# Optimization experiments

Hardware: AMD Instinct MI355X
Metric: run time of the kernel (lower is better)

Reference implementation:

```python
import jax, jax.numpy as jnp
import numpy as np

B, N, IN_DIM, H, D = 8, 128, 512, 8, 64  # batch, nodes, in_dim, heads, head_dim


def setup_inputs() -> dict:
    key = jax.random.key(0)
    ks = jax.random.split(key, 11)
    s = 0.02
    return {
        "h": jax.random.normal(ks[0], (B, N, IN_DIM), jnp.float32),
        "e": jax.random.normal(ks[1], (B, N, N, IN_DIM), jnp.float32),
        "k_RW": jax.random.uniform(ks[2], (B, N, N), jnp.float32),
        # Linear params stored as [in, out] (transpose of torch convention)
        "Wq": jax.random.normal(ks[3], (IN_DIM, H * D), jnp.float32) * s,
        "bq": jax.random.normal(ks[4], (H * D,), jnp.float32) * s,
        "Wk": jax.random.normal(ks[5], (IN_DIM, H * D), jnp.float32) * s,
        "bk": jax.random.normal(ks[6], (H * D,), jnp.float32) * s,
        "We": jax.random.normal(ks[7], (IN_DIM, H * D), jnp.float32) * s,
        "be": jax.random.normal(ks[8], (H * D,), jnp.float32) * s,
        "Wv": jax.random.normal(ks[9], (IN_DIM, H * D), jnp.float32) * s,
        "bv": jax.random.normal(ks[10], (H * D,), jnp.float32) * s,
    }


def reference(h, e, k_RW, Wq, bq, Wk, bk, We, be, Wv, bv):
    b, n = h.shape[0], h.shape[1]
    Q = (h @ Wq + bq).reshape(b, n, H, D)                       # bihd
    K = (h @ Wk + bk).reshape(b, n, H, D) * (float(D) ** -0.5)  # bjhd, scaled
    V = (h @ Wv + bv).reshape(b, n, H, D).transpose(0, 2, 1, 3)  # bhjd
    E = (e @ We + be).reshape(b, n, n, H, D)                    # bijhd
    # multiplicative edge-modulated attention scores
    scores = jnp.einsum('bihd,bjhd,bijhd->bhij', Q, K, E)
    scores = jnp.exp(jnp.clip(scores, -5.0, 5.0))
    scores = scores * k_RW[:, None, :, :]                       # adaptive edge PE
    denom = jnp.maximum(scores.sum(-1, keepdims=True), 1e-6)
    out = (scores @ V) / denom                                  # bhid
    return out.transpose(0, 2, 1, 3).reshape(b, n, H * D)
```

## Files before the change

kernel.cpp:

```cpp
#include <hip/hip_runtime.h>
#include <hip/hip_bf16.h>

#define BB    8
#define NNODE 128
#define CIN   512
#define HH    8
#define DDIM  64
#define HD    512

typedef float f32x4 __attribute__((ext_vector_type(4)));
typedef short bf16x8 __attribute__((ext_vector_type(8)));
typedef unsigned int u32x4 __attribute__((ext_vector_type(4)));

#define AS1 __attribute__((address_space(1)))
#define AS3 __attribute__((address_space(3)))

static __device__ __forceinline__ unsigned short f2bf(float f) {
    unsigned int x = __float_as_uint(f);
    x = x + 0x7FFFu + ((x >> 16) & 1u);
    return (unsigned short)(x >> 16);
}

static __device__ __forceinline__ bf16x8 pack8(f32x4 a, f32x4 b) {
    bf16x8 r;
    r[0] = (short)f2bf(a[0]); r[1] = (short)f2bf(a[1]);
    r[2] = (short)f2bf(a[2]); r[3] = (short)f2bf(a[3]);
    r[4] = (short)f2bf(b[0]); r[5] = (short)f2bf(b[1]);
    r[6] = (short)f2bf(b[2]); r[7] = (short)f2bf(b[3]);
    return r;
}

static __device__ __forceinline__ bf16x8 cvt8(f32x4 a, f32x4 b) {
    union { u32x4 u; bf16x8 h8; } cv;
    asm("v_cvt_pk_bf16_f32 %0, %1, %2" : "=v"(cv.u[0]) : "v"(a[0]), "v"(a[1]));
    asm("v_cvt_pk_bf16_f32 %0, %1, %2" : "=v"(cv.u[1]) : "v"(a[2]), "v"(a[3]));
    asm("v_cvt_pk_bf16_f32 %0, %1, %2" : "=v"(cv.u[2]) : "v"(b[0]), "v"(b[1]));
    asm("v_cvt_pk_bf16_f32 %0, %1, %2" : "=v"(cv.u[3]) : "v"(b[2]), "v"(b[3]));
    return cv.h8;
}

__global__ __launch_bounds__(256) void k_wt(
    const float* __restrict__ Wq, const float* __restrict__ Wk,
    const float* __restrict__ Wv,
    unsigned short* __restrict__ WT)
{
    __shared__ unsigned short tile[64][72];
    const int cb = blockIdx.x;
    const int hb = blockIdx.y;
    const int m  = blockIdx.z;
    const float* W = (m == 0) ? Wq : (m == 1) ? Wk : Wv;
    const int t = threadIdx.x;

#pragma unroll
    for (int it = 0; it < 4; ++it) {
        int row = it * 16 + (t >> 4);
        int col = (t & 15) * 4;
        f32x4 v = *reinterpret_cast<const f32x4*>(W + (size_t)(cb * 64 + row) * HD + hb * 64 + col);
        tile[row][col + 0] = f2bf(v[0]);
        tile[row][col + 1] = f2bf(v[1]);
        tile[row][col + 2] = f2bf(v[2]);
        tile[row][col + 3] = f2bf(v[3]);
    }
    __syncthreads();

#pragma unroll
    for (int it = 0; it < 4; ++it) {
        int hd = it * 16 + (t >> 4);
        int c  = (t & 15) * 4;
        unsigned long long pk =
            (unsigned long long)(unsigned short)tile[c + 0][hd] |
            ((unsigned long long)(unsigned short)tile[c + 1][hd] << 16) |
            ((unsigned long long)(unsigned short)tile[c + 2][hd] << 32) |
            ((unsigned long long)(unsigned short)tile[c + 3][hd] << 48);
        *reinterpret_cast<unsigned long long*>(
            &WT[((size_t)(m + 1) * HD + hb * 64 + hd) * CIN + cb * 64 + c]) = pk;
    }
}

__global__ __launch_bounds__(256) void k_qkv(
    const float* __restrict__ hin,
    const unsigned short* __restrict__ WT,
    const float* __restrict__ bq, const float* __restrict__ bk, const float* __restrict__ bv,
    float* __restrict__ Qo, float* __restrict__ Ko, float* __restrict__ Vo)
{
    __shared__ unsigned short hs[64][520];
    const int rt = blockIdx.x;
    const int ct = blockIdx.y;
    const int m  = blockIdx.z;
    const int t  = threadIdx.x;
    const int w  = t >> 6;
    const int l  = t & 63;
    const int g  = l >> 4;
    const int c15 = l & 15;
    const float* bias = (m == 0) ? bq : (m == 1) ? bk : bv;
    float* Out = (m == 0) ? Qo : (m == 1) ? Ko : Vo;
    const unsigned short* Wm = WT + (size_t)(m + 1) * HD * CIN;
    const int rowbase = rt * 64;
    const int colbase = ct * 64;

#pragma unroll
    for (int q = 0; q < 32; ++q) {
        int f = q * 1024 + t * 4;
        int row = f >> 9;
        int c = f & 511;
        f32x4 hv = *reinterpret_cast<const f32x4*>(hin + (size_t)(rowbase + row) * CIN + c);
        unsigned long long pk =
            (unsigned long long)f2bf(hv[0]) |
            ((unsigned long long)f2bf(hv[1]) << 16) |
            ((unsigned long long)f2bf(hv[2]) << 32) |
            ((unsigned long long)f2bf(hv[3]) << 48);
        *reinterpret_cast<unsigned long long*>(&hs[row][c]) = pk;
    }
    __syncthreads();

    f32x4 acc[4];
#pragma unroll
    for (int nf = 0; nf < 4; ++nf) acc[nf] = (f32x4){0.f, 0.f, 0.f, 0.f};

#pragma unroll
    for (int kt = 0; kt < 16; ++kt) {
        bf16x8 afr = *reinterpret_cast<const bf16x8*>(&hs[w * 16 + c15][kt * 32 + g * 8]);
#pragma unroll
        for (int nf = 0; nf < 4; ++nf) {
            const unsigned short* wp = Wm + (size_t)(colbase + nf * 16 + c15) * CIN + kt * 32 + g * 8;
            bf16x8 bfr = *reinterpret_cast<const bf16x8*>(wp);
            acc[nf] = __builtin_amdgcn_mfma_f32_16x16x32_bf16(afr, bfr, acc[nf], 0, 0, 0);
        }
    }

    const float scale = (m == 1) ? 0.125f : 1.0f;
#pragma unroll
    for (int nf = 0; nf < 4; ++nf) {
        int col = colbase + nf * 16 + c15;
        float bv_ = bias[col];
#pragma unroll
        for (int r = 0; r < 4; ++r) {
            int row = rowbase + w * 16 + g * 4 + r;
            Out[(size_t)row * HD + col] = (acc[nf][r] + bv_) * scale;
        }
    }
}

__global__ __launch_bounds__(256) void k_wtb(
    const float* __restrict__ We, unsigned short* __restrict__ WTB)
{
    const int h  = blockIdx.x;
    const int ct = blockIdx.y;
    const int t  = threadIdx.x;
#pragma unroll
    for (int it = 0; it < 2; ++it) {
        int s  = it * 256 + t;
        int kt = s >> 8, nf = (s >> 6) & 3, l = s & 63;
        int c0 = ct * 64 + kt * 32 + (l >> 4) * 8;
        int hd = h * 64 + nf * 16 + (l & 15);
        bf16x8 v;
#pragma unroll
        for (int i = 0; i < 8; ++i)
            v[i] = (short)f2bf(We[(size_t)(c0 + i) * HD + hd]);
        size_t off = ((size_t)(h * 8 + ct) * 8 + kt * 4 + nf) * 512 + l * 8;
        *reinterpret_cast<bf16x8*>(&WTB[off]) = v;
    }
}

__global__ __launch_bounds__(512, 1) void k_main(
    const float* __restrict__ e, const float* __restrict__ k_RW,
    const unsigned short* __restrict__ WTB, const float* __restrict__ be,
    const float* __restrict__ Qw, const float* __restrict__ Kw,
    const float* __restrict__ Vw, float* __restrict__ out)
{
    __shared__ float e_s[3 * 8192];
    __shared__ float s_lds[8][128];

    const int bx = blockIdx.x;
    const int bi = (bx & 7) * 128 + (bx >> 3);
    const int b  = bi >> 7;
    const int t  = threadIdx.x;
    const int h  = t >> 6;
    const int l  = t & 63;
    const int g  = l >> 4;
    const int c15 = l & 15;

    const float* ebase = e + (size_t)bi * NNODE * CIN;

    float q_l[4], be_l[4];
#pragma unroll
    for (int nf = 0; nf < 4; ++nf) {
        q_l[nf]  = Qw[(size_t)bi * HD + h * 64 + nf * 16 + c15];
        be_l[nf] = be[h * 64 + nf * 16 + c15];
    }

    f32x4 acc[8][4];
#pragma unroll
    for (int mf = 0; mf < 8; ++mf)
#pragma unroll
        for (int nf = 0; nf < 4; ++nf)
            acc[mf][nf] = (f32x4){0.f, 0.f, 0.f, 0.f};

    const int s00 = (((g * 2) + 0) ^ c15) << 4;
    const int s01 = (((g * 2) + 1) ^ c15) << 4;
    const int s10 = ((8 + (g * 2) + 0) ^ c15) << 4;
    const int s11 = ((8 + (g * 2) + 1) ^ c15) << 4;

#define STAGE(TT) do {                                                          \
        _Pragma("unroll")                                                       \
        for (int q_ = 0; q_ < 4; ++q_) {                                        \
            const int key_ = q_ * 4 + g;                                        \
            const float* src_ = ebase + (size_t)(h * 16 + key_) * CIN           \
                                + (TT) * 64 + ((c15 ^ key_) << 2);              \
            __builtin_amdgcn_global_load_lds(                                   \
                (const AS1 unsigned int*)src_,                                  \
                (AS3 unsigned int*)((char*)&e_s[0] + ((TT) % 3) * 32768         \
                                    + h * 4096 + q_ * 1024), 16, 0, 0);         \
        }                                                                       \
    } while (0)

#define LOADB(CT, B) do {                                                       \
        const unsigned short* bp_ = WTB + ((size_t)(h * 8 + (CT)) * 8) * 512 + l * 8; \
        _Pragma("unroll")                                                       \
        for (int f_ = 0; f_ < 8; ++f_)                                          \
            B[f_] = *reinterpret_cast<const bf16x8*>(bp_ + f_ * 512);           \
    } while (0)

#define COMPUTE(CT, BC) do {                                                    \
        const char* ebuf_ = (const char*)&e_s[0] + ((CT) % 3) * 32768;          \
        _Pragma("unroll")                                                       \
        for (int mf_ = 0; mf_ < 8; ++mf_) {                                     \
            const char* rp_ = ebuf_ + (mf_ * 16 + c15) * 256;                   \
            bf16x8 a0_ = cvt8(*(const f32x4*)(rp_ + s00),                       \
                              *(const f32x4*)(rp_ + s01));                      \
            bf16x8 a1_ = cvt8(*(const f32x4*)(rp_ + s10),                       \
                              *(const f32x4*)(rp_ + s11));                      \
            _Pragma("unroll")                                                   \
            for (int nf_ = 0; nf_ < 4; ++nf_) {                                 \
                acc[mf_][nf_] = __builtin_amdgcn_mfma_f32_16x16x32_bf16(        \
                    a0_, BC[nf_], acc[mf_][nf_], 0, 0, 0);                      \
                acc[mf_][nf_] = __builtin_amdgcn_mfma_f32_16x16x32_bf16(        \
                    a1_, BC[4 + nf_], acc[mf_][nf_], 0, 0, 0);                  \
            }                                                                   \
        }                                                                       \
    } while (0)

#define PHASE(CT, BC, BN) do {                                                  \
        if ((CT) < 7) { asm volatile("s_waitcnt vmcnt(4)" ::: "memory"); }      \
        else          { asm volatile("s_waitcnt vmcnt(0)" ::: "memory"); }      \
        __builtin_amdgcn_sched_barrier(0);                                      \
        __builtin_amdgcn_s_barrier();                                           \
        __builtin_amdgcn_sched_barrier(0);                                      \
        if ((CT) < 7) { LOADB((CT) + 1, BN); }                                  \
        __builtin_amdgcn_sched_barrier(0);                                      \
        if ((CT) < 6) { STAGE((CT) + 2); }                                      \
        __builtin_amdgcn_sched_barrier(0);                                      \
        COMPUTE(CT, BC);                                                        \
    } while (0)

    bf16x8 B0[8], B1[8];

    STAGE(0);
    LOADB(0, B0);
    STAGE(1);
    __builtin_amdgcn_sched_barrier(0);

    PHASE(0, B0, B1);
    PHASE(1, B1, B0);
    PHASE(2, B0, B1);
    PHASE(3, B1, B0);
    PHASE(4, B0, B1);
    PHASE(5, B1, B0);
    PHASE(6, B0, B1);
    PHASE(7, B1, B0);
#undef PHASE
#undef COMPUTE
#undef LOADB
#undef STAGE

    const float* Kb  = Kw + (size_t)b * NNODE * HD;
    const float* krw = k_RW + (size_t)bi * NNODE;
#pragma unroll
    for (int mf = 0; mf < 8; ++mf) {
#pragma unroll
        for (int r = 0; r < 4; ++r) {
            int j = mf * 16 + g * 4 + r;
            float s = 0.f;
#pragma unroll
            for (int nf = 0; nf < 4; ++nf) {
                float kv = Kb[(size_t)j * HD + h * 64 + nf * 16 + c15];
                s += (acc[mf][nf][r] + be_l[nf]) * q_l[nf] * kv;
            }
            s += __shfl_xor(s, 1);
            s += __shfl_xor(s, 2);
            s += __shfl_xor(s, 4);
            s += __shfl_xor(s, 8);
            if (c15 == 0)
                s_lds[h][j] = __expf(fminf(fmaxf(s, -5.f), 5.f)) * krw[j];
        }
    }

    const float* Vb = Vw + (size_t)b * NNODE * HD + h * 64 + l;
    float o = 0.f, den = 0.f;
#pragma unroll 4
    for (int jl = 0; jl < NNODE; ++jl) {
        float sv = s_lds[h][jl];
        o = fmaf(sv, Vb[(size_t)jl * HD], o);
        den += sv;
    }
    out[(size_t)bi * HD + h * 64 + l] = o / fmaxf(den, 1e-6f);
}

extern "C" void kernel_launch(void* const* d_in, const int* in_sizes, int n_in,
                              void* d_out, int out_size, void* d_ws, size_t ws_size,
                              hipStream_t stream) {
    const float* hin = (const float*)d_in[0];
    const float* e   = (const float*)d_in[1];
    const float* krw = (const float*)d_in[2];
    const float* Wq  = (const float*)d_in[3];
    const float* bq  = (const float*)d_in[4];
    const float* Wk  = (const float*)d_in[5];
    const float* bk  = (const float*)d_in[6];
    const float* We  = (const float*)d_in[7];
    const float* be  = (const float*)d_in[8];
    const float* Wv  = (const float*)d_in[9];
    const float* bv  = (const float*)d_in[10];
    float* out = (float*)d_out;

    char* ws = (char*)d_ws;
    unsigned short* WT  = (unsigned short*)ws;
    float* Q  = (float*)(ws + (2ull << 20));
    float* K  = (float*)(ws + (4ull << 20));
    float* V  = (float*)(ws + (6ull << 20));
    unsigned short* WTB = (unsigned short*)(ws + (8ull << 20));

    k_wt  <<<dim3(8, 8, 3), dim3(256), 0, stream>>>(Wq, Wk, Wv, WT);
    k_wtb <<<dim3(8, 8),    dim3(256), 0, stream>>>(We, WTB);
    k_qkv <<<dim3(16, 8, 3), dim3(256), 0, stream>>>(hin, WT, bq, bk, bv, Q, K, V);
    k_main<<<dim3(1024), dim3(512), 0, stream>>>(e, krw, WTB, be, Q, K, V, out);
}
```

Before: 220.3 us.

## Split main kernel over key halves with partial sums and normalization pass

Each (b,i) row is now handled by two blocks, each covering 64 of the 128 key nodes. Smaller LDS staging and fewer accumulators allow two blocks per CU. The blocks write partial numerators and denominators, and a new k_norm kernel combines them. The We B-fragment load drops from double buffering to a single buffer loaded within each phase, which exposes its latency. The change aims to raise occupancy and hide the memory stream of e, at the cost of an extra launch and a small workspace round-trip.

```diff
diff --git a/kernel.cpp b/kernel.cpp
--- a/kernel.cpp
+++ b/kernel.cpp
@@ -19,15 +19,6 @@
     unsigned int x = __float_as_uint(f);
     x = x + 0x7FFFu + ((x >> 16) & 1u);
     return (unsigned short)(x >> 16);
-}
-
-static __device__ __forceinline__ bf16x8 pack8(f32x4 a, f32x4 b) {
-    bf16x8 r;
-    r[0] = (short)f2bf(a[0]); r[1] = (short)f2bf(a[1]);
-    r[2] = (short)f2bf(a[2]); r[3] = (short)f2bf(a[3]);
-    r[4] = (short)f2bf(b[0]); r[5] = (short)f2bf(b[1]);
-    r[6] = (short)f2bf(b[2]); r[7] = (short)f2bf(b[3]);
-    return r;
 }
 
 static __device__ __forceinline__ bf16x8 cvt8(f32x4 a, f32x4 b) {
@@ -162,69 +153,63 @@
     }
 }
 
-__global__ __launch_bounds__(512, 1) void k_main(
+__global__ __launch_bounds__(512, 2) void k_main(
     const float* __restrict__ e, const float* __restrict__ k_RW,
     const unsigned short* __restrict__ WTB, const float* __restrict__ be,
     const float* __restrict__ Qw, const float* __restrict__ Kw,
-    const float* __restrict__ Vw, float* __restrict__ out)
-{
-    __shared__ float e_s[3 * 8192];
-    __shared__ float s_lds[8][128];
-
-    const int bx = blockIdx.x;
-    const int bi = (bx & 7) * 128 + (bx >> 3);
-    const int b  = bi >> 7;
-    const int t  = threadIdx.x;
-    const int h  = t >> 6;
-    const int l  = t & 63;
-    const int g  = l >> 4;
-    const int c15 = l & 15;
-
-    const float* ebase = e + (size_t)bi * NNODE * CIN;
-
-    float q_l[4], be_l[4];
-#pragma unroll
-    for (int nf = 0; nf < 4; ++nf) {
-        q_l[nf]  = Qw[(size_t)bi * HD + h * 64 + nf * 16 + c15];
-        be_l[nf] = be[h * 64 + nf * 16 + c15];
-    }
-
-    f32x4 acc[8][4];
-#pragma unroll
-    for (int mf = 0; mf < 8; ++mf)
+    const float* __restrict__ Vw, float* __restrict__ PN, float* __restrict__ PD)
+{
+    __shared__ float e_s[3 * 4096];
+    __shared__ float s_lds[8][64];
+
+    const int bx   = blockIdx.x;
+    const int bi   = bx >> 1;
+    const int half = bx & 1;
+    const int b    = bi >> 7;
+    const int t    = threadIdx.x;
+    const int h    = t >> 6;
+    const int l    = t & 63;
+    const int g    = l >> 4;
+    const int c15  = l & 15;
+
+    const float* ebase = e + ((size_t)bi * NNODE + half * 64) * CIN;
+
+    f32x4 acc[4][4];
+#pragma unroll
+    for (int mf = 0; mf < 4; ++mf)
 #pragma unroll
         for (int nf = 0; nf < 4; ++nf)
             acc[mf][nf] = (f32x4){0.f, 0.f, 0.f, 0.f};
 
-    const int s00 = (((g * 2) + 0) ^ c15) << 4;
-    const int s01 = (((g * 2) + 1) ^ c15) << 4;
-    const int s10 = ((8 + (g * 2) + 0) ^ c15) << 4;
-    const int s11 = ((8 + (g * 2) + 1) ^ c15) << 4;
+    const int s00 = ((g * 2 + 0) ^ c15) << 4;
+    const int s01 = ((g * 2 + 1) ^ c15) << 4;
+    const int s10 = ((8 + g * 2 + 0) ^ c15) << 4;
+    const int s11 = ((8 + g * 2 + 1) ^ c15) << 4;
 
 #define STAGE(TT) do {                                                          \
         _Pragma("unroll")                                                       \
-        for (int q_ = 0; q_ < 4; ++q_) {                                        \
-            const int key_ = q_ * 4 + g;                                        \
-            const float* src_ = ebase + (size_t)(h * 16 + key_) * CIN           \
+        for (int q_ = 0; q_ < 2; ++q_) {                                        \
+            const int key_ = ((h & 1) << 3) + q_ * 4 + g;                       \
+            const float* src_ = ebase + (size_t)(h * 8 + q_ * 4 + g) * CIN      \
                                 + (TT) * 64 + ((c15 ^ key_) << 2);              \
             __builtin_amdgcn_global_load_lds(                                   \
                 (const AS1 unsigned int*)src_,                                  \
-                (AS3 unsigned int*)((char*)&e_s[0] + ((TT) % 3) * 32768         \
-                                    + h * 4096 + q_ * 1024), 16, 0, 0);         \
+                (AS3 unsigned int*)((char*)&e_s[0] + ((TT) % 3) * 16384         \
+                                    + h * 2048 + q_ * 1024), 16, 0, 0);         \
         }                                                                       \
     } while (0)
 
-#define LOADB(CT, B) do {                                                       \
+#define LOADB(CT) do {                                                          \
         const unsigned short* bp_ = WTB + ((size_t)(h * 8 + (CT)) * 8) * 512 + l * 8; \
         _Pragma("unroll")                                                       \
         for (int f_ = 0; f_ < 8; ++f_)                                          \
-            B[f_] = *reinterpret_cast<const bf16x8*>(bp_ + f_ * 512);           \
+            wB[f_] = *reinterpret_cast<const bf16x8*>(bp_ + f_ * 512);          \
     } while (0)
 
-#define COMPUTE(CT, BC) do {                                                    \
-        const char* ebuf_ = (const char*)&e_s[0] + ((CT) % 3) * 32768;          \
+#define COMPUTE(CT) do {                                                        \
+        const char* ebuf_ = (const char*)&e_s[0] + ((CT) % 3) * 16384;          \
         _Pragma("unroll")                                                       \
-        for (int mf_ = 0; mf_ < 8; ++mf_) {                                     \
+        for (int mf_ = 0; mf_ < 4; ++mf_) {                                     \
             const char* rp_ = ebuf_ + (mf_ * 16 + c15) * 256;                   \
             bf16x8 a0_ = cvt8(*(const f32x4*)(rp_ + s00),                       \
                               *(const f32x4*)(rp_ + s01));                      \
@@ -233,57 +218,64 @@
             _Pragma("unroll")                                                   \
             for (int nf_ = 0; nf_ < 4; ++nf_) {                                 \
                 acc[mf_][nf_] = __builtin_amdgcn_mfma_f32_16x16x32_bf16(        \
-                    a0_, BC[nf_], acc[mf_][nf_], 0, 0, 0);                      \
+                    a0_, wB[nf_], acc[mf_][nf_], 0, 0, 0);                      \
                 acc[mf_][nf_] = __builtin_amdgcn_mfma_f32_16x16x32_bf16(        \
-                    a1_, BC[4 + nf_], acc[mf_][nf_], 0, 0, 0);                  \
+                    a1_, wB[4 + nf_], acc[mf_][nf_], 0, 0, 0);                  \
             }                                                                   \
         }                                                                       \
     } while (0)
 
-#define PHASE(CT, BC, BN) do {                                                  \
-        if ((CT) < 7) { asm volatile("s_waitcnt vmcnt(4)" ::: "memory"); }      \
+#define PHASE(CT) do {                                                          \
+        asm volatile("s_waitcnt vmcnt(2)" ::: "memory");                        \
+        __builtin_amdgcn_sched_barrier(0);                                      \
+        __builtin_amdgcn_s_barrier();                                           \
+        __builtin_amdgcn_sched_barrier(0);                                      \
+        LOADB(CT);                                                              \
+        __builtin_amdgcn_sched_barrier(0);                                      \
+        if ((CT) < 6) { STAGE((CT) + 2); }                                      \
+        __builtin_amdgcn_sched_barrier(0);                                      \
+        if ((CT) < 6) { asm volatile("s_waitcnt vmcnt(2)" ::: "memory"); }      \
         else          { asm volatile("s_waitcnt vmcnt(0)" ::: "memory"); }      \
         __builtin_amdgcn_sched_barrier(0);                                      \
-        __builtin_amdgcn_s_barrier();                                           \
-        __builtin_amdgcn_sched_barrier(0);                                      \
-        if ((CT) < 7) { LOADB((CT) + 1, BN); }                                  \
-        __builtin_amdgcn_sched_barrier(0);                                      \
-        if ((CT) < 6) { STAGE((CT) + 2); }                                      \
-        __builtin_amdgcn_sched_barrier(0);                                      \
-        COMPUTE(CT, BC);                                                        \
+        COMPUTE(CT);                                                            \
     } while (0)
 
-    bf16x8 B0[8], B1[8];
+    bf16x8 wB[8];
 
     STAGE(0);
-    LOADB(0, B0);
     STAGE(1);
     __builtin_amdgcn_sched_barrier(0);
 
-    PHASE(0, B0, B1);
-    PHASE(1, B1, B0);
-    PHASE(2, B0, B1);
-    PHASE(3, B1, B0);
-    PHASE(4, B0, B1);
-    PHASE(5, B1, B0);
-    PHASE(6, B0, B1);
-    PHASE(7, B1, B0);
+    PHASE(0);
+    PHASE(1);
+    PHASE(2);
+    PHASE(3);
+    PHASE(4);
+    PHASE(5);
+    PHASE(6);
+    PHASE(7);
 #undef PHASE
 #undef COMPUTE
 #undef LOADB
 #undef STAGE
 
-    const float* Kb  = Kw + (size_t)b * NNODE * HD;
-    const float* krw = k_RW + (size_t)bi * NNODE;
-#pragma unroll
-    for (int mf = 0; mf < 8; ++mf) {
+    float q_l[4], be_l[4];
+#pragma unroll
+    for (int nf = 0; nf < 4; ++nf) {
+        q_l[nf]  = Qw[(size_t)bi * HD + h * 64 + nf * 16 + c15];
+        be_l[nf] = be[h * 64 + nf * 16 + c15];
+    }
+    const float* Kb  = Kw + ((size_t)b * NNODE + half * 64) * HD;
+    const float* krw = k_RW + (size_t)bi * NNODE + half * 64;
+#pragma unroll
+    for (int mf = 0; mf < 4; ++mf) {
 #pragma unroll
         for (int r = 0; r < 4; ++r) {
-            int j = mf * 16 + g * 4 + r;
+            int jl = mf * 16 + g * 4 + r;
             float s = 0.f;
 #pragma unroll
             for (int nf = 0; nf < 4; ++nf) {
-                float kv = Kb[(size_t)j * HD + h * 64 + nf * 16 + c15];
+                float kv = Kb[(size_t)jl * HD + h * 64 + nf * 16 + c15];
                 s += (acc[mf][nf][r] + be_l[nf]) * q_l[nf] * kv;
             }
             s += __shfl_xor(s, 1);
@@ -291,19 +283,35 @@
             s += __shfl_xor(s, 4);
             s += __shfl_xor(s, 8);
             if (c15 == 0)
-                s_lds[h][j] = __expf(fminf(fmaxf(s, -5.f), 5.f)) * krw[j];
+                s_lds[h][jl] = __expf(fminf(fmaxf(s, -5.f), 5.f)) * krw[jl];
         }
     }
 
-    const float* Vb = Vw + (size_t)b * NNODE * HD + h * 64 + l;
+    const float* Vb = Vw + ((size_t)b * NNODE + half * 64) * HD + h * 64 + l;
     float o = 0.f, den = 0.f;
 #pragma unroll 4
-    for (int jl = 0; jl < NNODE; ++jl) {
+    for (int jl = 0; jl < 64; ++jl) {
         float sv = s_lds[h][jl];
         o = fmaf(sv, Vb[(size_t)jl * HD], o);
         den += sv;
     }
-    out[(size_t)bi * HD + h * 64 + l] = o / fmaxf(den, 1e-6f);
+    PN[((size_t)bx * 8 + h) * 64 + l] = o;
+    if (l == 0) PD[(size_t)bx * 8 + h] = den;
+}
+
+__global__ __launch_bounds__(512) void k_norm(
+    const float* __restrict__ PN, const float* __restrict__ PD,
+    float* __restrict__ out)
+{
+    const int bi = blockIdx.x;
+    const int t  = threadIdx.x;
+    const int h  = t >> 6;
+    const int d  = t & 63;
+    size_t r0 = ((size_t)(bi * 2 + 0) * 8 + h);
+    size_t r1 = ((size_t)(bi * 2 + 1) * 8 + h);
+    float num = PN[r0 * 64 + d] + PN[r1 * 64 + d];
+    float den = fmaxf(PD[r0] + PD[r1], 1e-6f);
+    out[(size_t)bi * HD + h * 64 + d] = num / den;
 }
 
 extern "C" void kernel_launch(void* const* d_in, const int* in_sizes, int n_in,
@@ -328,9 +336,12 @@
     float* K  = (float*)(ws + (4ull << 20));
     float* V  = (float*)(ws + (6ull << 20));
     unsigned short* WTB = (unsigned short*)(ws + (8ull << 20));
+    float* PN = (float*)(ws + (9ull << 20));
+    float* PD = (float*)(ws + (13ull << 20));
 
     k_wt  <<<dim3(8, 8, 3), dim3(256), 0, stream>>>(Wq, Wk, Wv, WT);
     k_wtb <<<dim3(8, 8),    dim3(256), 0, stream>>>(We, WTB);
     k_qkv <<<dim3(16, 8, 3), dim3(256), 0, stream>>>(hin, WT, bq, bk, bv, Q, K, V);
-    k_main<<<dim3(1024), dim3(512), 0, stream>>>(e, krw, WTB, be, Q, K, V, out);
-}
+    k_main<<<dim3(2048), dim3(512), 0, stream>>>(e, krw, WTB, be, Q, K, V, PN, PD);
+    k_norm<<<dim3(1024), dim3(512), 0, stream>>>(PN, PD, out);
+}
```

Result: slower. 236.9 us (+7.5%).
